# Performance work log

Hardware: AMD Instinct MI355X
Metric: run time of the kernel (lower is better)

The kernel has to match this reference:

```python
import jax, jax.numpy as jnp
import numpy as np

B, T, C, H = 4, 2048, 1024, 1024

def setup_inputs() -> dict:
    key = jax.random.key(0)
    ks = jax.random.split(key, 7)
    s = 0.02
    return {
        "x": jax.random.normal(ks[0], (B, T, C), dtype=jnp.float32),
        "k": jax.random.normal(ks[1], (B, T, C), dtype=jnp.float32),
        "q": jax.random.normal(ks[2], (B, T, C), dtype=jnp.float32),
        "v": jax.random.normal(ks[3], (B, T, C), dtype=jnp.float32),
        "Wk": jax.random.normal(ks[4], (C, H), dtype=jnp.float32) * s,
        "Wq": jax.random.normal(ks[5], (C, H), dtype=jnp.float32) * s,
        "Wv": jax.random.normal(ks[6], (C, H), dtype=jnp.float32) * s,
    }

def reference(x, k, q, v, Wk, Wq, Wv):
    Tcur = x.shape[1]
    kp = jnp.einsum('btc,ch->bth', k, Wk)
    qp = jnp.einsum('btc,ch->bth', q, Wq)
    # NOTE: original torch code (faithfully) projects v with the QUERY weights
    vp = jnp.einsum('btc,ch->bth', v, Wq)
    scale = jnp.asarray(H, jnp.float32) ** -0.5
    weights = jnp.einsum('bth,bsh->bts', qp, kp) * scale  # [B,T,T]
    causal = jnp.tril(jnp.ones((Tcur, Tcur), dtype=bool))
    weights = jnp.where(causal, weights, -jnp.inf)
    weights = jax.nn.softmax(weights, axis=-1)
    # dropout p=0.0 -> identity
    out = jnp.einsum('bts,bsh->bth', weights, vp)
    return out
```

## Files before the change

kernel.cpp:

```cpp
#include <hip/hip_runtime.h>
#include <stdint.h>

typedef unsigned short u16;
typedef __attribute__((ext_vector_type(8))) short short8;
typedef __attribute__((ext_vector_type(8))) u16 ushort8;
typedef __attribute__((ext_vector_type(4))) u16 u16x4;
typedef __attribute__((ext_vector_type(4))) float floatx4;

__device__ __forceinline__ u16 f2bf(float f) {
  union { float f; unsigned u; } c; c.f = f;
  unsigned u = c.u;
  return (u16)((u + 0x7fffu + ((u >> 16) & 1u)) >> 16);
}
__device__ __forceinline__ float bf2f(u16 h) {
  union { unsigned u; float f; } c; c.u = (unsigned)h << 16;
  return c.f;
}

__device__ __forceinline__ void async16(const u16* g, u16* l) {
  auto* gp = reinterpret_cast<const __attribute__((address_space(1))) uint32_t*>(
      reinterpret_cast<uintptr_t>(g));
  auto* lp = reinterpret_cast<__attribute__((address_space(3))) uint32_t*>(
      reinterpret_cast<uintptr_t>(l));
  __builtin_amdgcn_global_load_lds(gp, lp, 16, 0, 0);
}

template <int OUT_BF16>
__global__ __launch_bounds__(256) void gemm_bt(
    const u16* __restrict__ A, const u16* __restrict__ B, void* __restrict__ Cv,
    int K, int lda, int ldb, int ldc,
    long long sA, long long sB, long long sC,
    float scale, int causal_skip, int causal_klimit,
    int vpt, u16* __restrict__ vpC) {
  const int m0 = blockIdx.x * 128;
  const int n0 = blockIdx.y * 128;
  if (causal_skip && n0 >= m0 + 128) return;
  A += (size_t)blockIdx.z * sA;
  B += (size_t)blockIdx.z * sB;

  __shared__ u16 As[128 * 32];
  __shared__ u16 Bs[128 * 32];

  const int tid = threadIdx.x;
  const int lane = tid & 63;
  const int wid = tid >> 6;
  const int wm = (wid & 1) * 64;
  const int wn = (wid >> 1) * 64;
  const int fr = lane & 15;
  const int fq = lane >> 4;

  floatx4 acc[4][4] = {};

  int kt_end = K >> 5;
  if (causal_klimit) {
    int lim = (m0 >> 5) + 4;
    if (lim < kt_end) kt_end = lim;
  }

  const int rowi = tid >> 2;
  const int segi = tid & 3;
  const int sgz = segi ^ ((rowi >> 1) & 3);
  const u16* gA = A + (size_t)(m0 + rowi) * lda + sgz * 8;
  const u16* gB = B + (size_t)(n0 + rowi) * ldb + sgz * 8;
  u16* lA = &As[tid * 8];
  u16* lB = &Bs[tid * 8];

  const u16* rdA[4];
  const u16* rdB[4];
#pragma unroll
  for (int i = 0; i < 4; ++i) {
    int ra = wm + i * 16 + fr;
    rdA[i] = &As[ra * 32 + (fq ^ ((ra >> 1) & 3)) * 8];
    int rb = wn + i * 16 + fr;
    rdB[i] = &Bs[rb * 32 + (fq ^ ((rb >> 1) & 3)) * 8];
  }

  for (int kt = 0; kt < kt_end; ++kt) {
    const int k0 = kt << 5;
    async16(gA + k0, lA);
    async16(gA + k0 + (size_t)64 * lda, lA + 2048);
    async16(gB + k0, lB);
    async16(gB + k0 + (size_t)64 * ldb, lB + 2048);
    __builtin_amdgcn_s_waitcnt(0);
    __syncthreads();

    short8 av[4], bv[4];
#pragma unroll
    for (int i = 0; i < 4; ++i) av[i] = *(const short8*)rdA[i];
#pragma unroll
    for (int j = 0; j < 4; ++j) bv[j] = *(const short8*)rdB[j];

#pragma unroll
    for (int i = 0; i < 4; ++i)
#pragma unroll
      for (int j = 0; j < 4; ++j)
        acc[i][j] = __builtin_amdgcn_mfma_f32_16x16x32_bf16(av[i], bv[j],
                                                            acc[i][j], 0, 0, 0);
    __syncthreads();
  }

  if (vpt && blockIdx.z == 2) {
#pragma unroll
    for (int i = 0; i < 4; ++i) {
      const int m = m0 + wm + i * 16 + fq * 4;
      const int b = m >> 11, t = m & 2047;
#pragma unroll
      for (int j = 0; j < 4; ++j) {
        const int n = n0 + wn + j * 16 + fr;
        u16x4 o;
#pragma unroll
        for (int r = 0; r < 4; ++r) o[r] = f2bf(acc[i][j][r]);
        *(u16x4*)&vpC[(size_t)b * 2097152 + (size_t)n * 2048 + t] = o;
      }
    }
    return;
  }
  if (OUT_BF16) {
    u16* C = (u16*)Cv + (size_t)blockIdx.z * sC;
#pragma unroll
    for (int i = 0; i < 4; ++i) {
      const int m = m0 + wm + i * 16 + fq * 4;
#pragma unroll
      for (int j = 0; j < 4; ++j) {
        const int n = n0 + wn + j * 16 + fr;
#pragma unroll
        for (int r = 0; r < 4; ++r)
          C[(size_t)(m + r) * ldc + n] = f2bf(acc[i][j][r] * scale);
      }
    }
  } else {
    float* C = (float*)Cv + (size_t)blockIdx.z * sC;
#pragma unroll
    for (int i = 0; i < 4; ++i) {
      const int m = m0 + wm + i * 16 + fq * 4;
#pragma unroll
      for (int j = 0; j < 4; ++j) {
        const int n = n0 + wn + j * 16 + fr;
#pragma unroll
        for (int r = 0; r < 4; ++r)
          C[(size_t)(m + r) * ldc + n] = acc[i][j][r] * scale;
      }
    }
  }
}

__global__ __launch_bounds__(256) void cast3(
    const float* __restrict__ q, const float* __restrict__ k,
    const float* __restrict__ v, u16* __restrict__ out, int n8) {
  int i = blockIdx.x * 256 + threadIdx.x;
  if (i >= n8) return;
  const float* src = blockIdx.y == 0 ? q : (blockIdx.y == 1 ? k : v);
  u16* dst = out + (size_t)blockIdx.y * n8 * 8;
  floatx4 a = ((const floatx4*)src)[i * 2];
  floatx4 b = ((const floatx4*)src)[i * 2 + 1];
  ushort8 o;
#pragma unroll
  for (int j = 0; j < 4; ++j) { o[j] = f2bf(a[j]); o[4 + j] = f2bf(b[j]); }
  ((ushort8*)dst)[i] = o;
}

__global__ __launch_bounds__(256) void transpose_castW(
    const float* __restrict__ Wq, const float* __restrict__ Wk,
    u16* __restrict__ out, int R, int C) {
  __shared__ u16 tile[64][72];
  const float* in = (blockIdx.z == 1) ? Wk : Wq;
  u16* dst = out + (size_t)blockIdx.z * R * C;
  const int r0 = blockIdx.x * 64;
  const int c0 = blockIdx.y * 64;
  const int tid = threadIdx.x;
#pragma unroll
  for (int rnd = 0; rnd < 2; ++rnd) {
    int e = rnd * 256 + tid;
    int rr = e >> 3, seg = e & 7;
    const float* p = &in[(size_t)(r0 + rr) * C + c0 + seg * 8];
    floatx4 a = *(const floatx4*)p;
    floatx4 b = *(const floatx4*)(p + 4);
    u16* tp = &tile[rr][seg * 8];
#pragma unroll
    for (int j = 0; j < 4; ++j) { tp[j] = f2bf(a[j]); tp[4 + j] = f2bf(b[j]); }
  }
  __syncthreads();
#pragma unroll
  for (int rnd = 0; rnd < 2; ++rnd) {
    int e = rnd * 256 + tid;
    int cc = e >> 3, rseg = e & 7;
    ushort8 tv;
#pragma unroll
    for (int j = 0; j < 8; ++j) tv[j] = tile[rseg * 8 + j][cc];
    *(ushort8*)&dst[(size_t)(c0 + cc) * R + r0 + rseg * 8] = tv;
  }
}

__global__ __launch_bounds__(256) void softmax_causal(u16* __restrict__ S,
                                                      int T) {
  const int row = blockIdx.x;
  const int t = row & (T - 1);
  const int len = t + 1;
  u16* srow = S + (size_t)row * T;
  const int tid = threadIdx.x;

  float vals[8];
  int cnt = 0;
  float mx = -1e30f;
  for (int i = tid; i < len; i += 256) {
    float v = bf2f(srow[i]);
    vals[cnt++] = v;
    mx = fmaxf(mx, v);
  }
  __shared__ float red[4];
#pragma unroll
  for (int o = 32; o > 0; o >>= 1) mx = fmaxf(mx, __shfl_down(mx, o, 64));
  if ((tid & 63) == 0) red[tid >> 6] = mx;
  __syncthreads();
  mx = fmaxf(fmaxf(red[0], red[1]), fmaxf(red[2], red[3]));
  __syncthreads();

  float sum = 0.f;
  for (int c = 0; c < cnt; ++c) {
    vals[c] = __expf(vals[c] - mx);
    sum += vals[c];
  }
#pragma unroll
  for (int o = 32; o > 0; o >>= 1) sum += __shfl_down(sum, o, 64);
  if ((tid & 63) == 0) red[tid >> 6] = sum;
  __syncthreads();
  sum = red[0] + red[1] + red[2] + red[3];
  const float inv = 1.f / sum;

  int c = 0;
  for (int i = tid; i < len; i += 256) srow[i] = f2bf(vals[c++] * inv);
  for (int i = tid; i < T; i += 256)
    if (i >= len) srow[i] = 0;
}

extern "C" void kernel_launch(void* const* d_in, const int* in_sizes, int n_in,
                              void* d_out, int out_size, void* d_ws,
                              size_t ws_size, hipStream_t stream) {
  (void)in_sizes; (void)n_in; (void)out_size; (void)ws_size;
  const float* k  = (const float*)d_in[1];
  const float* q  = (const float*)d_in[2];
  const float* v  = (const float*)d_in[3];
  const float* Wk = (const float*)d_in[4];
  const float* Wq = (const float*)d_in[5];
  float* out = (float*)d_out;

  const int B = 4, T = 2048, C = 1024, H = 1024;
  const int M = B * T;
  const size_t MC = (size_t)M * C, CH = (size_t)C * H, MH = (size_t)M * H;

  u16* qkv  = (u16*)d_ws;
  u16* WT   = qkv + 3 * MC;
  u16* qkvp = WT + 3 * CH;
  u16* vpT  = qkvp + 2 * MH;
  u16* Sb   = vpT + MH;

  const int n8 = (int)(MC / 8);
  cast3<<<dim3(n8 / 256, 3), 256, 0, stream>>>(q, k, v, qkv, n8);
  transpose_castW<<<dim3(C / 64, H / 64, 3), 256, 0, stream>>>(Wq, Wk, WT, C, H);

  gemm_bt<1><<<dim3(M / 128, H / 128, 3), 256, 0, stream>>>(
      qkv, WT, qkvp, C, C, C, H,
      (long long)MC, (long long)CH, (long long)MH, 1.f, 0, 0, 1, vpT);

  gemm_bt<1><<<dim3(T / 128, T / 128, B), 256, 0, stream>>>(
      qkvp, qkvp + MH, Sb, H, H, H, T,
      (long long)T * H, (long long)T * H, (long long)T * T,
      0.03125f, 1, 0, 0, nullptr);

  softmax_causal<<<dim3(B * T), 256, 0, stream>>>(Sb, T);

  gemm_bt<0><<<dim3(T / 128, H / 128, B), 256, 0, stream>>>(
      Sb, vpT, out, T, T, T, H,
      (long long)T * T, (long long)H * T, (long long)T * H,
      1.f, 0, 1, 0, nullptr);
}
```

Measured before the change: 359.6 us.

## Double-buffer GEMM LDS tiles, triangular grid for QK^T, reverse M order for PV

Converts the GEMM main loop to double-buffered LDS. The next K-tile's async global-to-LDS loads are issued before waiting on the current tile, so memory latency overlaps with MFMA work. The QK^T launch now enumerates only the lower-triangular 128x128 tiles (136 per batch) instead of launching and early-exiting the full grid. The causal PV GEMM schedules the longest rows first to reduce tail imbalance. Doubling LDS per block may reduce occupancy, and the raw waitcnt encodings depend on vmcnt semantics being correct.

```diff
diff --git a/kernel.cpp b/kernel.cpp
--- a/kernel.cpp
+++ b/kernel.cpp
@@ -1,5 +1,6 @@
 #include <hip/hip_runtime.h>
 #include <stdint.h>
+#include <math.h>
 
 typedef unsigned short u16;
 typedef __attribute__((ext_vector_type(8))) short short8;
@@ -25,21 +26,35 @@
   __builtin_amdgcn_global_load_lds(gp, lp, 16, 0, 0);
 }
 
+#define WAIT_VM4 0xF74
+#define WAIT_VM0 0xF70
+
 template <int OUT_BF16>
 __global__ __launch_bounds__(256) void gemm_bt(
     const u16* __restrict__ A, const u16* __restrict__ B, void* __restrict__ Cv,
     int K, int lda, int ldb, int ldc,
     long long sA, long long sB, long long sC,
-    float scale, int causal_skip, int causal_klimit,
+    float scale, int tri_grid, int causal_klimit, int rev_m,
     int vpt, u16* __restrict__ vpC) {
-  const int m0 = blockIdx.x * 128;
-  const int n0 = blockIdx.y * 128;
-  if (causal_skip && n0 >= m0 + 128) return;
+  int bm, bn;
+  if (tri_grid) {
+    const int bx = blockIdx.x;
+    int i = (int)((sqrtf(8.f * bx + 1.f) - 1.f) * 0.5f);
+    while ((i + 1) * (i + 2) / 2 <= bx) ++i;
+    while (i * (i + 1) / 2 > bx) --i;
+    bm = i;
+    bn = bx - i * (i + 1) / 2;
+  } else {
+    bm = rev_m ? ((int)gridDim.x - 1 - (int)blockIdx.x) : (int)blockIdx.x;
+    bn = blockIdx.y;
+  }
+  const int m0 = bm * 128;
+  const int n0 = bn * 128;
   A += (size_t)blockIdx.z * sA;
   B += (size_t)blockIdx.z * sB;
 
-  __shared__ u16 As[128 * 32];
-  __shared__ u16 Bs[128 * 32];
+  __shared__ u16 As[2][4096];
+  __shared__ u16 Bs[2][4096];
 
   const int tid = threadIdx.x;
   const int lane = tid & 63;
@@ -62,33 +77,42 @@
   const int sgz = segi ^ ((rowi >> 1) & 3);
   const u16* gA = A + (size_t)(m0 + rowi) * lda + sgz * 8;
   const u16* gB = B + (size_t)(n0 + rowi) * ldb + sgz * 8;
-  u16* lA = &As[tid * 8];
-  u16* lB = &Bs[tid * 8];
-
-  const u16* rdA[4];
-  const u16* rdB[4];
+
+  int offA[4], offB[4];
 #pragma unroll
   for (int i = 0; i < 4; ++i) {
     int ra = wm + i * 16 + fr;
-    rdA[i] = &As[ra * 32 + (fq ^ ((ra >> 1) & 3)) * 8];
+    offA[i] = ra * 32 + (fq ^ ((ra >> 1) & 3)) * 8;
     int rb = wn + i * 16 + fr;
-    rdB[i] = &Bs[rb * 32 + (fq ^ ((rb >> 1) & 3)) * 8];
-  }
-
+    offB[i] = rb * 32 + (fq ^ ((rb >> 1) & 3)) * 8;
+  }
+
+  auto issue = [&](int kt) {
+    const int k0 = kt << 5;
+    const int odd = kt & 1;
+    async16(gA + k0, &As[odd][tid * 8]);
+    async16(gA + k0 + (size_t)64 * lda, &As[odd][tid * 8 + 2048]);
+    async16(gB + k0, &Bs[odd][tid * 8]);
+    async16(gB + k0 + (size_t)64 * ldb, &Bs[odd][tid * 8 + 2048]);
+  };
+
+  issue(0);
   for (int kt = 0; kt < kt_end; ++kt) {
-    const int k0 = kt << 5;
-    async16(gA + k0, lA);
-    async16(gA + k0 + (size_t)64 * lda, lA + 2048);
-    async16(gB + k0, lB);
-    async16(gB + k0 + (size_t)64 * ldb, lB + 2048);
-    __builtin_amdgcn_s_waitcnt(0);
-    __syncthreads();
-
+    if (kt + 1 < kt_end) {
+      issue(kt + 1);
+      __builtin_amdgcn_s_waitcnt(WAIT_VM4);
+    } else {
+      __builtin_amdgcn_s_waitcnt(WAIT_VM0);
+    }
+    asm volatile("s_barrier" ::: "memory");
+
+    const u16* ab = As[kt & 1];
+    const u16* bb = Bs[kt & 1];
     short8 av[4], bv[4];
 #pragma unroll
-    for (int i = 0; i < 4; ++i) av[i] = *(const short8*)rdA[i];
-#pragma unroll
-    for (int j = 0; j < 4; ++j) bv[j] = *(const short8*)rdB[j];
+    for (int i = 0; i < 4; ++i) av[i] = *(const short8*)(ab + offA[i]);
+#pragma unroll
+    for (int j = 0; j < 4; ++j) bv[j] = *(const short8*)(bb + offB[j]);
 
 #pragma unroll
     for (int i = 0; i < 4; ++i)
@@ -96,7 +120,7 @@
       for (int j = 0; j < 4; ++j)
         acc[i][j] = __builtin_amdgcn_mfma_f32_16x16x32_bf16(av[i], bv[j],
                                                             acc[i][j], 0, 0, 0);
-    __syncthreads();
+    asm volatile("s_barrier" ::: "memory");
   }
 
   if (vpt && blockIdx.z == 2) {
@@ -260,17 +284,17 @@
 
   gemm_bt<1><<<dim3(M / 128, H / 128, 3), 256, 0, stream>>>(
       qkv, WT, qkvp, C, C, C, H,
-      (long long)MC, (long long)CH, (long long)MH, 1.f, 0, 0, 1, vpT);
-
-  gemm_bt<1><<<dim3(T / 128, T / 128, B), 256, 0, stream>>>(
+      (long long)MC, (long long)CH, (long long)MH, 1.f, 0, 0, 0, 1, vpT);
+
+  gemm_bt<1><<<dim3(136, 1, B), 256, 0, stream>>>(
       qkvp, qkvp + MH, Sb, H, H, H, T,
       (long long)T * H, (long long)T * H, (long long)T * T,
-      0.03125f, 1, 0, 0, nullptr);
+      0.03125f, 1, 0, 0, 0, nullptr);
 
   softmax_causal<<<dim3(B * T), 256, 0, stream>>>(Sb, T);
 
   gemm_bt<0><<<dim3(T / 128, H / 128, B), 256, 0, stream>>>(
       Sb, vpT, out, T, T, T, H,
       (long long)T * T, (long long)H * T, (long long)T * H,
-      1.f, 0, 1, 0, nullptr);
-}
+      1.f, 0, 1, 1, 0, nullptr);
+}
```

Result: faster. 332.1 us (-7.6%).
